# Performance work log

Hardware: AMD Instinct MI355X
Metric: run time of the kernel (lower is better)

Reference implementation:

```python
import jax, jax.numpy as jnp
import numpy as np

B, S, D, N, H = 2, 2048, 1024, 16, 64  # batch, seq, d_model, heads, depth


def setup_inputs() -> dict:
    key = jax.random.key(0)
    ks = jax.random.split(key, 7)
    scale = 1.0 / np.sqrt(D)
    # causal mask: 1.0 where attention is disallowed (future positions)
    mask = jnp.triu(jnp.ones((S, S), dtype=jnp.float32), k=1)[None, None]
    return {
        "v_input": jax.random.normal(ks[0], (B, S, D), dtype=jnp.float32),
        "k_input": jax.random.normal(ks[1], (B, S, D), dtype=jnp.float32),
        "q_input": jax.random.normal(ks[2], (B, S, D), dtype=jnp.float32),
        "mask": mask,
        "Wq": jax.random.normal(ks[3], (D, N, H), dtype=jnp.float32) * scale,
        "Wk": jax.random.normal(ks[4], (D, N, H), dtype=jnp.float32) * scale,
        "Wv": jax.random.normal(ks[5], (D, N, H), dtype=jnp.float32) * scale,
        "Wo": jax.random.normal(ks[6], (N, H, D), dtype=jnp.float32) * scale,
    }


def reference(v_input, k_input, q_input, mask, Wq, Wk, Wv, Wo):
    q = jnp.einsum("bfd,dnh->bfnh", q_input, Wq)
    k = jnp.einsum("btd,dnh->btnh", k_input, Wk)
    v = jnp.einsum("btd,dnh->btnh", v_input, Wv)
    dk = jnp.asarray(H, dtype=jnp.float32)
    logits = jnp.einsum("bfnh,btnh->bnft", q, k) / jnp.sqrt(dk)
    logits = logits + mask * -1e9
    attn = jax.nn.softmax(logits, axis=-1)  # [B, N, F, T]
    ctx = jnp.einsum("bnft,btnh->bfnh", attn, v)
    out = jnp.einsum("bfnh,nhd->bfd", ctx, Wo)
    return out, attn
```

## Files before the change

### kernel.cpp

```cpp
#include <hip/hip_runtime.h>
#include <hip/hip_bf16.h>
#include <cstdint>


typedef __attribute__((ext_vector_type(4))) float f32x4;
typedef __attribute__((ext_vector_type(8))) short s16x8;
typedef __attribute__((ext_vector_type(8))) unsigned short us8;
typedef __attribute__((ext_vector_type(4))) unsigned short us4;

#define MFMA16(a, b, c) __builtin_amdgcn_mfma_f32_16x16x32_bf16((a), (b), (c), 0, 0, 0)
constexpr float L2E = 1.4426950408889634f;

__device__ __forceinline__ unsigned short f2bf(float f) {
  unsigned int u = __builtin_bit_cast(unsigned int, f);
  u += 0x7FFFu + ((u >> 16) & 1u);
  return (unsigned short)(u >> 16);
}
__device__ __forceinline__ unsigned int cvtpk(float lo, float hi) {
  unsigned int r;
  asm("v_cvt_pk_bf16_f32 %0, %1, %2" : "=v"(r) : "v"(lo), "v"(hi));
  return r;
}
__device__ __forceinline__ s16x8 ldfrag(const unsigned short* p) {
  return __builtin_bit_cast(s16x8, *(const us8*)p);
}
__device__ __forceinline__ void gload16(const void* g, void* l) {
  auto* gp = reinterpret_cast<const __attribute__((address_space(1))) unsigned int*>(
      reinterpret_cast<uintptr_t>(g));
  auto* lp = reinterpret_cast<__attribute__((address_space(3))) unsigned int*>(
      reinterpret_cast<uintptr_t>(l));
  __builtin_amdgcn_global_load_lds(gp, lp, 16, 0, 0);
}

__global__ __launch_bounds__(256) void convin_k(const float* __restrict__ s0,
                                                const float* __restrict__ s1,
                                                const float* __restrict__ s2,
                                                unsigned short* __restrict__ d0,
                                                unsigned short* __restrict__ d1,
                                                unsigned short* __restrict__ d2) {
  const float* s = blockIdx.y == 0 ? s0 : (blockIdx.y == 1 ? s1 : s2);
  unsigned short* d = blockIdx.y == 0 ? d0 : (blockIdx.y == 1 ? d1 : d2);
  int gid = blockIdx.x * 256 + threadIdx.x;
  int m = gid >> 7, kg = gid & 127;
  f32x4 a = *(const f32x4*)(s + (size_t)m * 1024 + kg * 8);
  f32x4 b = *(const f32x4*)(s + (size_t)m * 1024 + kg * 8 + 4);
  us8 o;
#pragma unroll
  for (int j = 0; j < 4; ++j) { o[j] = f2bf(a[j]); o[j + 4] = f2bf(b[j]); }
  int kgp = (kg & ~7) | ((kg ^ m) & 7);
  *(us8*)(d + (size_t)m * 1024 + kgp * 8) = o;
}

__global__ __launch_bounds__(256) void convw_k(const float* __restrict__ w0,
                                               const float* __restrict__ w1,
                                               const float* __restrict__ w2,
                                               const float* __restrict__ w3,
                                               unsigned short* __restrict__ o0,
                                               unsigned short* __restrict__ o1,
                                               unsigned short* __restrict__ o2,
                                               unsigned short* __restrict__ o3) {
  const float* W = blockIdx.y == 0 ? w0 : (blockIdx.y == 1 ? w1 : (blockIdx.y == 2 ? w2 : w3));
  unsigned short* O = blockIdx.y == 0 ? o0 : (blockIdx.y == 1 ? o1 : (blockIdx.y == 2 ? o2 : o3));
  const int t = threadIdx.x;
  const int r0 = (blockIdx.x & 15) * 64, c0 = (blockIdx.x >> 4) * 64;
  __shared__ float tile[64][65];
  {
    int r = t >> 2, cq = (t & 3) * 16;
#pragma unroll
    for (int j = 0; j < 4; ++j) {
      f32x4 v = *(const f32x4*)(W + (size_t)(r0 + r) * 1024 + c0 + cq + j * 4);
#pragma unroll
      for (int e = 0; e < 4; ++e) tile[r][cq + j * 4 + e] = v[e];
    }
  }
  __syncthreads();
  int orow = t >> 2;
  int gr = c0 + orow;
#pragma unroll
  for (int gi = 0; gi < 2; ++gi) {
    int dl = (t & 3) * 16 + gi * 8;
    us8 o;
#pragma unroll
    for (int j = 0; j < 8; ++j) o[j] = f2bf(tile[dl + j][orow]);
    int kg = (r0 + dl) >> 3;
    int kgp = (kg & ~7) | ((kg ^ gr) & 7);
    *(us8*)(O + (size_t)gr * 1024 + kgp * 8) = o;
  }
}

__global__ __launch_bounds__(256) void qkv_gemm(
    const unsigned short* __restrict__ Aq, const unsigned short* __restrict__ Ak,
    const unsigned short* __restrict__ Av, const unsigned short* __restrict__ Bq,
    const unsigned short* __restrict__ Bk, const unsigned short* __restrict__ Bv,
    unsigned short* __restrict__ Oq, unsigned short* __restrict__ Ok,
    unsigned short* __restrict__ Ov) {
  const int z = blockIdx.z;
  const unsigned short* A = z == 0 ? Aq : (z == 1 ? Ak : Av);
  const unsigned short* Bt = z == 0 ? Bq : (z == 1 ? Bk : Bv);

  __shared__ __align__(16) unsigned short lds[16384];
  const int t = threadIdx.x, w = t >> 6, lane = t & 63;
  const int lr = lane & 15, lg = lane >> 4;
  const int wr = (w >> 1) * 64, wc = (w & 1) * 64;
  const int m0 = blockIdx.y * 128, n0 = blockIdx.x * 128;
  const int srow = w * 32 + (lane >> 3), sg = lane & 7;

  f32x4 acc[4][4];
#pragma unroll
  for (int i = 0; i < 4; ++i)
#pragma unroll
    for (int j = 0; j < 4; ++j) acc[i][j] = (f32x4){0.f, 0.f, 0.f, 0.f};

  for (int k0 = 0; k0 < 1024; k0 += 64) {
#pragma unroll
    for (int q = 0; q < 4; ++q)
      gload16(A + (size_t)(m0 + srow + q * 8) * 1024 + k0 + sg * 8,
              &lds[(w * 32 + q * 8) * 64]);
#pragma unroll
    for (int q = 0; q < 4; ++q)
      gload16(Bt + (size_t)(n0 + srow + q * 8) * 1024 + k0 + sg * 8,
              &lds[8192 + (w * 32 + q * 8) * 64]);
    __syncthreads();
#pragma unroll
    for (int r2 = 0; r2 < 2; ++r2) {
      const int koff = ((r2 * 4 + lg) ^ (lr & 7)) * 8;
      s16x8 af[4], bfr[4];
#pragma unroll
      for (int x = 0; x < 4; ++x) af[x] = ldfrag(&lds[(wr + x * 16 + lr) * 64 + koff]);
#pragma unroll
      for (int x = 0; x < 4; ++x) bfr[x] = ldfrag(&lds[8192 + (wc + x * 16 + lr) * 64 + koff]);
#pragma unroll
      for (int am = 0; am < 4; ++am)
#pragma unroll
        for (int bn = 0; bn < 4; ++bn) acc[am][bn] = MFMA16(af[am], bfr[bn], acc[am][bn]);
    }
    __syncthreads();
  }

  if (z < 2) {
    unsigned short* C = z == 0 ? Oq : Ok;
    const float scale = z == 0 ? 0.125f : 1.0f;
#pragma unroll
    for (int am = 0; am < 4; ++am)
#pragma unroll
      for (int bn = 0; bn < 4; ++bn)
#pragma unroll
        for (int i = 0; i < 4; ++i) {
          int gr = m0 + wr + am * 16 + lg * 4 + i;
          int gc = n0 + wc + bn * 16 + lr;
          int bb = gr >> 11, ss = gr & 2047;
          int nn = gc >> 6, hh = gc & 63;
          size_t base = ((size_t)(bb * 16 + nn)) * 131072 + (size_t)(ss >> 6) * 4096;
          int off = ((ss >> 4) & 3) * 1024 + (hh >> 5) * 512 +
                    (((hh >> 3) & 3) * 16 + (ss & 15)) * 8 + (hh & 7);
          C[base + off] = f2bf(acc[am][bn][i] * scale);
        }
  } else {
#pragma unroll
    for (int am = 0; am < 4; ++am)
#pragma unroll
      for (int bn = 0; bn < 4; ++bn)
#pragma unroll
        for (int i = 0; i < 4; ++i) {
          int gr = m0 + wr + am * 16 + lg * 4 + i;
          int gc = n0 + wc + bn * 16 + lr;
          int bb = gr >> 11, ss = gr & 2047;
          int nn = gc >> 6, hh = gc & 63;
          size_t base = ((size_t)(bb * 16 + nn)) * 131072 + (size_t)(ss >> 6) * 4096;
          int off = hh * 64 + (((((ss >> 3) & 7) ^ (hh & 7))) << 3) + (ss & 7);
          Ov[base + off] = f2bf(acc[am][bn][i]);
        }
  }
}

__global__ __launch_bounds__(256) void gemmWo(const unsigned short* __restrict__ A,
                                              const unsigned short* __restrict__ Bt,
                                              float* __restrict__ C) {
  __shared__ __align__(16) unsigned short lds[12288];
  const int t = threadIdx.x, w = t >> 6, lane = t & 63;
  const int lr = lane & 15, lg = lane >> 4;
  const int wr = (w >> 1) * 64, wc = (w & 1) * 32;
  const int m0 = blockIdx.y * 128, n0 = blockIdx.x * 64;

  f32x4 acc[4][2];
#pragma unroll
  for (int i = 0; i < 4; ++i)
#pragma unroll
    for (int j = 0; j < 2; ++j) acc[i][j] = (f32x4){0.f, 0.f, 0.f, 0.f};

  for (int k0 = 0; k0 < 1024; k0 += 64) {
#pragma unroll
    for (int q = 0; q < 4; ++q)
      gload16(A + (size_t)(m0 + w * 32 + q * 8 + (lane >> 3)) * 1024 + k0 + (lane & 7) * 8,
              &lds[(w * 32 + q * 8) * 64]);
#pragma unroll
    for (int q = 0; q < 2; ++q)
      gload16(Bt + (size_t)(n0 + w * 16 + q * 8 + (lane >> 3)) * 1024 + k0 + (lane & 7) * 8,
              &lds[8192 + (w * 16 + q * 8) * 64]);
    __syncthreads();
#pragma unroll
    for (int r2 = 0; r2 < 2; ++r2) {
      const int koff = ((r2 * 4 + lg) ^ (lr & 7)) * 8;
      s16x8 af[4], bfr[2];
#pragma unroll
      for (int x = 0; x < 4; ++x) af[x] = ldfrag(&lds[(wr + x * 16 + lr) * 64 + koff]);
#pragma unroll
      for (int x = 0; x < 2; ++x) bfr[x] = ldfrag(&lds[8192 + (wc + x * 16 + lr) * 64 + koff]);
#pragma unroll
      for (int am = 0; am < 4; ++am)
#pragma unroll
        for (int bn = 0; bn < 2; ++bn) acc[am][bn] = MFMA16(af[am], bfr[bn], acc[am][bn]);
    }
    __syncthreads();
  }
#pragma unroll
  for (int am = 0; am < 4; ++am)
#pragma unroll
    for (int bn = 0; bn < 2; ++bn)
#pragma unroll
      for (int i = 0; i < 4; ++i) {
        int gr = m0 + wr + am * 16 + lg * 4 + i;
        int gc = n0 + wc + bn * 16 + lr;
        C[(size_t)gr * 1024 + gc] = acc[am][bn][i];
      }
}

__global__ __launch_bounds__(256) void attn_k(const unsigned short* __restrict__ qw,
                                              const unsigned short* __restrict__ kw,
                                              const unsigned short* __restrict__ vw,
                                              float* __restrict__ attn,
                                              unsigned short* __restrict__ ctx) {
  constexpr int S = 2048, N = 16;
  const int flat = blockIdx.x;
  const int nf = (flat & 7) * 128 + (flat >> 3);
  const int qt = 31 - (nf & 31);
  const int hd = (nf >> 5) & 15, b = nf >> 9;
  const int qbase = qt * 64;
  const int t = threadIdx.x, w = t >> 6, lane = t & 63;
  const int lr = lane & 15, lg = lane >> 4;
  const size_t headoff = ((size_t)(b * N + hd)) * S * 64;
  const unsigned short* qh = qw + headoff;
  const unsigned short* kh = kw + headoff;
  const unsigned short* vh = vw + headoff;
  float* attn_h = attn + ((size_t)(b * N + hd)) * S * S;
  const int qrow = qbase + w * 16 + lr;

  __shared__ __align__(16) unsigned short ldsv[2][4096];
  __shared__ __align__(16) float twbuf[4][16][72];

  s16x8 qf0 = ldfrag(qh + (size_t)qt * 4096 + w * 1024 + lane * 8);
  s16x8 qf1 = ldfrag(qh + (size_t)qt * 4096 + w * 1024 + 512 + lane * 8);

  s16x8 kA[8], kB[8];
  auto loadK = [&](s16x8(&kf)[8], int kt) {
    const unsigned short* kb = kh + (size_t)kt * 4096;
#pragma unroll
    for (int fc = 0; fc < 4; ++fc) {
      kf[fc * 2] = ldfrag(kb + fc * 1024 + lane * 8);
      kf[fc * 2 + 1] = ldfrag(kb + fc * 1024 + 512 + lane * 8);
    }
  };

  float lsum = 0.f;
  auto p1body = [&](s16x8(&kf)[8], int kt) {
    float ts = 0.f;
#pragma unroll
    for (int fc = 0; fc < 4; ++fc) {
      f32x4 a = (f32x4){0.f, 0.f, 0.f, 0.f};
      a = MFMA16(kf[fc * 2], qf0, a);
      a = MFMA16(kf[fc * 2 + 1], qf1, a);
      if (kt == qt) {
#pragma unroll
        for (int i = 0; i < 4; ++i)
          if (qbase + fc * 16 + lg * 4 + i > qrow) a[i] = -3.0e38f;
      }
#pragma unroll
      for (int i = 0; i < 4; ++i) ts += __builtin_amdgcn_exp2f(a[i] * L2E);
    }
    lsum += ts;
  };
  loadK(kA, 0);
  {
    int kt = 0;
    while (true) {
      if (kt < qt) loadK(kB, kt + 1);
      p1body(kA, kt);
      if (++kt > qt) break;
      if (kt < qt) loadK(kA, kt + 1);
      p1body(kB, kt);
      if (++kt > qt) break;
    }
  }
  lsum += __shfl_xor(lsum, 16);
  lsum += __shfl_xor(lsum, 32);
  const float c0 = -__builtin_amdgcn_logf(lsum);

  f32x4 accpv[4];
#pragma unroll
  for (int i = 0; i < 4; ++i) accpv[i] = (f32x4){0.f, 0.f, 0.f, 0.f};
  const int src0 = lr + 32 * (lg & 1), src1 = src0 + 16;
  const bool hiFc = (lg >> 1) & 1;

  auto vdma = [&](int kt, int buf) {
    const unsigned short* vsrc = vh + (size_t)kt * 4096;
    gload16(vsrc + (w * 128 + lane) * 8, &ldsv[buf][w * 1024]);
    gload16(vsrc + (w * 128 + 64 + lane) * 8, &ldsv[buf][w * 1024 + 512]);
  };

  auto p2body = [&](s16x8(&kf)[8], int kt) {
    const int cb = kt & 1;
    f32x4 s[4];
#pragma unroll
    for (int fc = 0; fc < 4; ++fc) {
      f32x4 a = (f32x4){0.f, 0.f, 0.f, 0.f};
      a = MFMA16(kf[fc * 2], qf0, a);
      a = MFMA16(kf[fc * 2 + 1], qf1, a);
      s[fc] = a;
    }
    unsigned int Wlo[4], Whi[4];
#pragma unroll
    for (int fc = 0; fc < 4; ++fc) {
      f32x4 p;
#pragma unroll
      for (int i = 0; i < 4; ++i)
        p[i] = __builtin_amdgcn_exp2f(__builtin_fmaf(s[fc][i], L2E, c0));
      if (kt == qt) {
#pragma unroll
        for (int i = 0; i < 4; ++i)
          if (qbase + fc * 16 + lg * 4 + i > qrow) p[i] = 0.0f;
      }
      *(f32x4*)&twbuf[w][lr][fc * 16 + lg * 4] = p;
      Wlo[fc] = cvtpk(p[0], p[1]);
      Whi[fc] = cvtpk(p[2], p[3]);
    }
#pragma unroll
    for (int ks = 0; ks < 2; ++ks) {
      unsigned int d0a = __shfl((int)Wlo[2 * ks], src0, 64);
      unsigned int d0b = __shfl((int)Wlo[2 * ks + 1], src0, 64);
      unsigned int d1a = __shfl((int)Whi[2 * ks], src0, 64);
      unsigned int d1b = __shfl((int)Whi[2 * ks + 1], src0, 64);
      unsigned int d2a = __shfl((int)Wlo[2 * ks], src1, 64);
      unsigned int d2b = __shfl((int)Wlo[2 * ks + 1], src1, 64);
      unsigned int d3a = __shfl((int)Whi[2 * ks], src1, 64);
      unsigned int d3b = __shfl((int)Whi[2 * ks + 1], src1, 64);
      unsigned int pd[4] = {hiFc ? d0b : d0a, hiFc ? d1b : d1a,
                            hiFc ? d2b : d2a, hiFc ? d3b : d3a};
      s16x8 pa = __builtin_bit_cast(s16x8, *(us8*)pd);
#pragma unroll
      for (int hc = 0; hc < 4; ++hc) {
        s16x8 vb = ldfrag(&ldsv[cb][(hc * 16 + lr) * 64 + (((ks * 4 + lg) ^ (lr & 7)) << 3)]);
        accpv[hc] = MFMA16(pa, vb, accpv[hc]);
      }
    }
#pragma unroll
    for (int rr = 0; rr < 4; ++rr) {
      f32x4 v = *(const f32x4*)&twbuf[w][lg * 4 + rr][lr * 4];
      __builtin_nontemporal_store(
          v, (f32x4*)(attn_h + (size_t)(qbase + w * 16 + lg * 4 + rr) * S + kt * 64 + lr * 4));
    }
  };

  loadK(kA, 0);
  vdma(0, 0);
  {
    int kt = 0;
    while (true) {
      __syncthreads();
      if (kt < qt) { vdma(kt + 1, (kt + 1) & 1); loadK(kB, kt + 1); }
      p2body(kA, kt);
      if (++kt > qt) break;
      __syncthreads();
      if (kt < qt) { vdma(kt + 1, (kt + 1) & 1); loadK(kA, kt + 1); }
      p2body(kB, kt);
      if (++kt > qt) break;
    }
  }

  const int zstart = (qt + 1) * 64;
  if (zstart < S) {
    const int n4 = (S - zstart) >> 2;
    const f32x4 z = (f32x4){0.f, 0.f, 0.f, 0.f};
    for (int r = 0; r < 64; ++r) {
      float* dst = attn_h + (size_t)(qbase + r) * S + zstart;
      for (int i = t; i < n4; i += 256)
        __builtin_nontemporal_store(z, (f32x4*)(dst + i * 4));
    }
  }

#pragma unroll
  for (int hc = 0; hc < 4; ++hc)
#pragma unroll
    for (int i = 0; i < 4; ++i) {
      int mr = b * S + qbase + w * 16 + lg * 4 + i;
      int nh = hd * 64 + hc * 16 + lr;
      int kg = nh >> 3, el = nh & 7;
      int kgp = (kg & ~7) | ((kg ^ mr) & 7);
      ctx[(size_t)mr * 1024 + kgp * 8 + el] = f2bf(accpv[hc][i]);
    }
}

extern "C" void kernel_launch(void* const* d_in, const int* in_sizes, int n_in,
                              void* d_out, int out_size, void* d_ws, size_t ws_size,
                              hipStream_t stream) {
  (void)in_sizes; (void)n_in; (void)out_size; (void)ws_size;
  const float* v_in = (const float*)d_in[0];
  const float* k_in = (const float*)d_in[1];
  const float* q_in = (const float*)d_in[2];
  const float* Wq = (const float*)d_in[4];
  const float* Wk = (const float*)d_in[5];
  const float* Wv = (const float*)d_in[6];
  const float* Wo = (const float*)d_in[7];

  float* out = (float*)d_out;
  float* attn = out + (size_t)2 * 2048 * 1024;

  unsigned short* ws = (unsigned short*)d_ws;
  const size_t MK = (size_t)4096 * 1024;
  const size_t WK = (size_t)1024 * 1024;
  unsigned short* qbfA = ws;
  unsigned short* kbfA = ws + MK;
  unsigned short* vbfA = ws + 2 * MK;
  unsigned short* WqT = ws + 3 * MK;
  unsigned short* WkT = WqT + WK;
  unsigned short* WvT = WkT + WK;
  unsigned short* WoT = WvT + WK;
  unsigned short* q_ws = WoT + WK;
  unsigned short* k_ws = q_ws + MK;
  unsigned short* v_ws = k_ws + MK;
  unsigned short* ctx_ws = v_ws + MK;

  convin_k<<<dim3(2048, 3), 256, 0, stream>>>(q_in, k_in, v_in, qbfA, kbfA, vbfA);
  convw_k<<<dim3(256, 4), 256, 0, stream>>>(Wq, Wk, Wv, Wo, WqT, WkT, WvT, WoT);

  qkv_gemm<<<dim3(8, 32, 3), 256, 0, stream>>>(qbfA, kbfA, vbfA, WqT, WkT, WvT,
                                               q_ws, k_ws, v_ws);
  attn_k<<<1024, 256, 0, stream>>>(q_ws, k_ws, v_ws, attn, ctx_ws);
  gemmWo<<<dim3(16, 32), 256, 0, stream>>>(ctx_ws, WoT, out);
}
```

Before: 212.7 us.

## Merge conversion kernels, stage QKV epilogue via LDS, remap GEMM blocks across XCDs

The two fp32-to-bf16 conversion kernels become one launch that branches on block index. The QKV GEMM epilogue now writes tiles into LDS in the head-major layout and then stores them to global memory as 16-byte vectors, replacing scattered 2-byte stores. Both GEMMs remap flat block indices so that neighbouring tiles land on the same XCD, for better L2 reuse. The Wo output uses nontemporal stores and the attention transpose buffer padding goes from 72 to 76 floats to change LDS bank mapping. These are several independent tweaks, and the LDS-staged epilogue adds an extra barrier.

```diff
diff --git a/kernel.cpp b/kernel.cpp
--- a/kernel.cpp
+++ b/kernel.cpp
@@ -32,59 +32,58 @@
   __builtin_amdgcn_global_load_lds(gp, lp, 16, 0, 0);
 }
 
-__global__ __launch_bounds__(256) void convin_k(const float* __restrict__ s0,
-                                                const float* __restrict__ s1,
-                                                const float* __restrict__ s2,
-                                                unsigned short* __restrict__ d0,
-                                                unsigned short* __restrict__ d1,
-                                                unsigned short* __restrict__ d2) {
-  const float* s = blockIdx.y == 0 ? s0 : (blockIdx.y == 1 ? s1 : s2);
-  unsigned short* d = blockIdx.y == 0 ? d0 : (blockIdx.y == 1 ? d1 : d2);
-  int gid = blockIdx.x * 256 + threadIdx.x;
-  int m = gid >> 7, kg = gid & 127;
-  f32x4 a = *(const f32x4*)(s + (size_t)m * 1024 + kg * 8);
-  f32x4 b = *(const f32x4*)(s + (size_t)m * 1024 + kg * 8 + 4);
-  us8 o;
-#pragma unroll
-  for (int j = 0; j < 4; ++j) { o[j] = f2bf(a[j]); o[j + 4] = f2bf(b[j]); }
-  int kgp = (kg & ~7) | ((kg ^ m) & 7);
-  *(us8*)(d + (size_t)m * 1024 + kgp * 8) = o;
-}
-
-__global__ __launch_bounds__(256) void convw_k(const float* __restrict__ w0,
-                                               const float* __restrict__ w1,
-                                               const float* __restrict__ w2,
-                                               const float* __restrict__ w3,
-                                               unsigned short* __restrict__ o0,
-                                               unsigned short* __restrict__ o1,
-                                               unsigned short* __restrict__ o2,
-                                               unsigned short* __restrict__ o3) {
-  const float* W = blockIdx.y == 0 ? w0 : (blockIdx.y == 1 ? w1 : (blockIdx.y == 2 ? w2 : w3));
-  unsigned short* O = blockIdx.y == 0 ? o0 : (blockIdx.y == 1 ? o1 : (blockIdx.y == 2 ? o2 : o3));
+__global__ __launch_bounds__(256) void conv_k(
+    const float* __restrict__ s0, const float* __restrict__ s1,
+    const float* __restrict__ s2, unsigned short* __restrict__ d0,
+    unsigned short* __restrict__ d1, unsigned short* __restrict__ d2,
+    const float* __restrict__ w0, const float* __restrict__ w1,
+    const float* __restrict__ w2, const float* __restrict__ w3,
+    unsigned short* __restrict__ o0, unsigned short* __restrict__ o1,
+    unsigned short* __restrict__ o2, unsigned short* __restrict__ o3) {
+  const int blk = blockIdx.x;
   const int t = threadIdx.x;
-  const int r0 = (blockIdx.x & 15) * 64, c0 = (blockIdx.x >> 4) * 64;
   __shared__ float tile[64][65];
-  {
-    int r = t >> 2, cq = (t & 3) * 16;
-#pragma unroll
-    for (int j = 0; j < 4; ++j) {
-      f32x4 v = *(const f32x4*)(W + (size_t)(r0 + r) * 1024 + c0 + cq + j * 4);
-#pragma unroll
-      for (int e = 0; e < 4; ++e) tile[r][cq + j * 4 + e] = v[e];
-    }
-  }
-  __syncthreads();
-  int orow = t >> 2;
-  int gr = c0 + orow;
-#pragma unroll
-  for (int gi = 0; gi < 2; ++gi) {
-    int dl = (t & 3) * 16 + gi * 8;
+  if (blk < 6144) {
+    const int y = blk >> 11, x = blk & 2047;
+    const float* s = y == 0 ? s0 : (y == 1 ? s1 : s2);
+    unsigned short* d = y == 0 ? d0 : (y == 1 ? d1 : d2);
+    int gid = x * 256 + t;
+    int m = gid >> 7, kg = gid & 127;
+    f32x4 a = *(const f32x4*)(s + (size_t)m * 1024 + kg * 8);
+    f32x4 b = *(const f32x4*)(s + (size_t)m * 1024 + kg * 8 + 4);
     us8 o;
 #pragma unroll
-    for (int j = 0; j < 8; ++j) o[j] = f2bf(tile[dl + j][orow]);
-    int kg = (r0 + dl) >> 3;
-    int kgp = (kg & ~7) | ((kg ^ gr) & 7);
-    *(us8*)(O + (size_t)gr * 1024 + kgp * 8) = o;
+    for (int j = 0; j < 4; ++j) { o[j] = f2bf(a[j]); o[j + 4] = f2bf(b[j]); }
+    int kgp = (kg & ~7) | ((kg ^ m) & 7);
+    *(us8*)(d + (size_t)m * 1024 + kgp * 8) = o;
+  } else {
+    const int r = blk - 6144;
+    const int y = r >> 8, x = r & 255;
+    const float* W = y == 0 ? w0 : (y == 1 ? w1 : (y == 2 ? w2 : w3));
+    unsigned short* O = y == 0 ? o0 : (y == 1 ? o1 : (y == 2 ? o2 : o3));
+    const int r0 = (x & 15) * 64, c0 = (x >> 4) * 64;
+    {
+      int rr = t >> 2, cq = (t & 3) * 16;
+#pragma unroll
+      for (int j = 0; j < 4; ++j) {
+        f32x4 v = *(const f32x4*)(W + (size_t)(r0 + rr) * 1024 + c0 + cq + j * 4);
+#pragma unroll
+        for (int e = 0; e < 4; ++e) tile[rr][cq + j * 4 + e] = v[e];
+      }
+    }
+    __syncthreads();
+    int orow = t >> 2;
+    int gr = c0 + orow;
+#pragma unroll
+    for (int gi = 0; gi < 2; ++gi) {
+      int dl = (t & 3) * 16 + gi * 8;
+      us8 o;
+#pragma unroll
+      for (int j = 0; j < 8; ++j) o[j] = f2bf(tile[dl + j][orow]);
+      int kg = (r0 + dl) >> 3;
+      int kgp = (kg & ~7) | ((kg ^ gr) & 7);
+      *(us8*)(O + (size_t)gr * 1024 + kgp * 8) = o;
+    }
   }
 }
 
@@ -102,7 +101,9 @@
   const int t = threadIdx.x, w = t >> 6, lane = t & 63;
   const int lr = lane & 15, lg = lane >> 4;
   const int wr = (w >> 1) * 64, wc = (w & 1) * 64;
-  const int m0 = blockIdx.y * 128, n0 = blockIdx.x * 128;
+  const int xf = blockIdx.x;
+  const int nfb = (xf & 7) * 32 + (xf >> 3);
+  const int m0 = (nfb >> 3) * 128, n0 = (nfb & 7) * 128;
   const int srow = w * 32 + (lane >> 3), sg = lane & 7;
 
   f32x4 acc[4][4];
@@ -137,39 +138,36 @@
     __syncthreads();
   }
 
-  if (z < 2) {
-    unsigned short* C = z == 0 ? Oq : Ok;
-    const float scale = z == 0 ? 0.125f : 1.0f;
-#pragma unroll
-    for (int am = 0; am < 4; ++am)
-#pragma unroll
-      for (int bn = 0; bn < 4; ++bn)
-#pragma unroll
-        for (int i = 0; i < 4; ++i) {
-          int gr = m0 + wr + am * 16 + lg * 4 + i;
-          int gc = n0 + wc + bn * 16 + lr;
-          int bb = gr >> 11, ss = gr & 2047;
-          int nn = gc >> 6, hh = gc & 63;
-          size_t base = ((size_t)(bb * 16 + nn)) * 131072 + (size_t)(ss >> 6) * 4096;
-          int off = ((ss >> 4) & 3) * 1024 + (hh >> 5) * 512 +
-                    (((hh >> 3) & 3) * 16 + (ss & 15)) * 8 + (hh & 7);
-          C[base + off] = f2bf(acc[am][bn][i] * scale);
-        }
-  } else {
-#pragma unroll
-    for (int am = 0; am < 4; ++am)
-#pragma unroll
-      for (int bn = 0; bn < 4; ++bn)
-#pragma unroll
-        for (int i = 0; i < 4; ++i) {
-          int gr = m0 + wr + am * 16 + lg * 4 + i;
-          int gc = n0 + wc + bn * 16 + lr;
-          int bb = gr >> 11, ss = gr & 2047;
-          int nn = gc >> 6, hh = gc & 63;
-          size_t base = ((size_t)(bb * 16 + nn)) * 131072 + (size_t)(ss >> 6) * 4096;
-          int off = hh * 64 + (((((ss >> 3) & 7) ^ (hh & 7))) << 3) + (ss & 7);
-          Ov[base + off] = f2bf(acc[am][bn][i]);
-        }
+  const float scale = z == 0 ? 0.125f : 1.0f;
+#pragma unroll
+  for (int am = 0; am < 4; ++am)
+#pragma unroll
+    for (int bn = 0; bn < 4; ++bn)
+#pragma unroll
+      for (int i = 0; i < 4; ++i) {
+        int grl = wr + am * 16 + lg * 4 + i;
+        int gcl = wc + bn * 16 + lr;
+        int st = grl >> 6, s6 = grl & 63;
+        int hd2 = gcl >> 6, h6 = gcl & 63;
+        int off;
+        if (z < 2)
+          off = ((s6 >> 4) & 3) * 1024 + (h6 >> 5) * 512 +
+                (((h6 >> 3) & 3) * 16 + (s6 & 15)) * 8 + (h6 & 7);
+        else
+          off = h6 * 64 + ((((s6 >> 3) & 7) ^ (h6 & 7)) << 3) + (s6 & 7);
+        lds[(st * 2 + hd2) * 4096 + off] = f2bf(acc[am][bn][i] * scale);
+      }
+  __syncthreads();
+  unsigned short* C = z == 0 ? Oq : (z == 1 ? Ok : Ov);
+  const int bb = m0 >> 11, t0 = (m0 & 2047) >> 6, nn0 = n0 >> 6;
+#pragma unroll
+  for (int c = 0; c < 8; ++c) {
+    int g = c * 256 + t;
+    int sub = g >> 9, inner = g & 511;
+    int st = sub >> 1, hd2 = sub & 1;
+    size_t dst = ((size_t)(bb * 16 + nn0 + hd2)) * 131072 + (size_t)(t0 + st) * 4096 +
+                 (size_t)inner * 8;
+    *(us8*)(C + dst) = *(const us8*)&lds[g * 8];
   }
 }
 
@@ -180,7 +178,9 @@
   const int t = threadIdx.x, w = t >> 6, lane = t & 63;
   const int lr = lane & 15, lg = lane >> 4;
   const int wr = (w >> 1) * 64, wc = (w & 1) * 32;
-  const int m0 = blockIdx.y * 128, n0 = blockIdx.x * 64;
+  const int xf = blockIdx.x;
+  const int nfb = (xf & 7) * 64 + (xf >> 3);
+  const int m0 = (nfb >> 4) * 128, n0 = (nfb & 15) * 64;
 
   f32x4 acc[4][2];
 #pragma unroll
@@ -221,7 +221,7 @@
       for (int i = 0; i < 4; ++i) {
         int gr = m0 + wr + am * 16 + lg * 4 + i;
         int gc = n0 + wc + bn * 16 + lr;
-        C[(size_t)gr * 1024 + gc] = acc[am][bn][i];
+        __builtin_nontemporal_store(acc[am][bn][i], &C[(size_t)gr * 1024 + gc]);
       }
 }
 
@@ -246,7 +246,7 @@
   const int qrow = qbase + w * 16 + lr;
 
   __shared__ __align__(16) unsigned short ldsv[2][4096];
-  __shared__ __align__(16) float twbuf[4][16][72];
+  __shared__ __align__(16) float twbuf[4][16][76];
 
   s16x8 qf0 = ldfrag(qh + (size_t)qt * 4096 + w * 1024 + lane * 8);
   s16x8 qf1 = ldfrag(qh + (size_t)qt * 4096 + w * 1024 + 512 + lane * 8);
@@ -429,11 +429,10 @@
   unsigned short* v_ws = k_ws + MK;
   unsigned short* ctx_ws = v_ws + MK;
 
-  convin_k<<<dim3(2048, 3), 256, 0, stream>>>(q_in, k_in, v_in, qbfA, kbfA, vbfA);
-  convw_k<<<dim3(256, 4), 256, 0, stream>>>(Wq, Wk, Wv, Wo, WqT, WkT, WvT, WoT);
-
-  qkv_gemm<<<dim3(8, 32, 3), 256, 0, stream>>>(qbfA, kbfA, vbfA, WqT, WkT, WvT,
-                                               q_ws, k_ws, v_ws);
+  conv_k<<<7168, 256, 0, stream>>>(q_in, k_in, v_in, qbfA, kbfA, vbfA,
+                                   Wq, Wk, Wv, Wo, WqT, WkT, WvT, WoT);
+  qkv_gemm<<<dim3(256, 1, 3), 256, 0, stream>>>(qbfA, kbfA, vbfA, WqT, WkT, WvT,
+                                                q_ws, k_ws, v_ws);
   attn_k<<<1024, 256, 0, stream>>>(q_ws, k_ws, v_ws, attn, ctx_ws);
-  gemmWo<<<dim3(16, 32), 256, 0, stream>>>(ctx_ws, WoT, out);
-}
+  gemmWo<<<512, 256, 0, stream>>>(ctx_ws, WoT, out);
+}
```

After: 208.1 us. 2.2% less time.
